# Kernel tuning notes

Hardware: AMD Instinct MI355X
Metric: run time of the kernel (lower is better)

Reference implementation:

```python
import jax, jax.numpy as jnp
import numpy as np

K = 20          # neighbors
EPS = 1e-5      # BatchNorm eps
SLOPE = 0.2     # LeakyReLU negative slope


def setup_inputs() -> dict:
    key = jax.random.key(0)
    k1, k2 = jax.random.split(key)
    B, C, N, O = 8, 64, 4096, 64
    x = jax.random.normal(k1, (B, C, N), dtype=jnp.float32)
    # 1x1 Conv2d(2C -> O, bias=False) kernel, squeezed to (O, 2C)
    W = jax.random.normal(k2, (O, 2 * C), dtype=jnp.float32) * 0.05
    gamma = jnp.ones((O,), jnp.float32)   # BN weight
    beta = jnp.zeros((O,), jnp.float32)   # BN bias
    return {"x": x, "W": W, "gamma": gamma, "beta": beta}


def _edgeconv(x, W, gamma, beta):
    B, C, N = x.shape
    xt = jnp.transpose(x, (0, 2, 1))                       # (B, N, C)
    # KNN on negative squared distance (matches torch topk of -dist)
    xx = jnp.sum(x * x, axis=1)                            # (B, N)
    inner = jnp.einsum('bnc,bmc->bnm', xt, xt)             # (B, N, N)
    neg_dist = 2.0 * inner - xx[:, :, None] - xx[:, None, :]
    _, idx = jax.lax.top_k(neg_dist, K)                    # (B, N, K) int32
    # gather neighbor features: nbr[b,n,k,c] = xt[b, idx[b,n,k], c]
    nbr = xt[jnp.arange(B)[:, None, None], idx]            # (B, N, K, C)
    center = jnp.broadcast_to(xt[:, :, None, :], (B, N, K, C))
    edge = jnp.concatenate([nbr - center, center], axis=-1)  # (B, N, K, 2C)
    # 1x1 conv == channel matmul
    y = jnp.einsum('bnkc,oc->bnko', edge, W)               # (B, N, K, O)
    # BatchNorm2d (training mode: batch statistics over B,N,K per channel)
    mean = jnp.mean(y, axis=(0, 1, 2))
    var = jnp.var(y, axis=(0, 1, 2))
    yn = (y - mean) * jax.lax.rsqrt(var + EPS) * gamma + beta
    ya = jnp.where(yn >= 0, yn, SLOPE * yn)                # LeakyReLU(0.2)
    out = jnp.max(ya, axis=2)                              # max over k -> (B, N, O)
    return jnp.transpose(out, (0, 2, 1))                   # (B, O, N)


def reference(x, W, gamma, beta):
    return _edgeconv(x, W, gamma, beta)
```

## Files before the change

### kernel.cpp

```cpp
#include <hip/hip_runtime.h>
#include <hip/hip_bf16.h>
#include <math.h>

#define B 8
#define C 64
#define NN 4096
#define O 64
#define KNN 20

typedef float f32x4 __attribute__((ext_vector_type(4)));
typedef short short8_t __attribute__((ext_vector_type(8)));

__device__ inline uint32_t fkey(float f) {
    uint32_t u = __float_as_uint(f);
    return u ^ (((uint32_t)((int32_t)u >> 31)) | 0x80000000u);
}

__device__ inline uint32_t med3u(uint32_t a, uint32_t b, uint32_t c) {
    uint32_t r;
    asm("v_med3_u32 %0, %1, %2, %3" : "=v"(r) : "v"(a), "v"(b), "v"(c));
    return r;
}
__device__ inline uint32_t umax(uint32_t a, uint32_t b) { return a > b ? a : b; }
__device__ inline uint32_t umin(uint32_t a, uint32_t b) { return a < b ? a : b; }

__device__ inline uint32_t maxall16(uint32_t v) {
    uint32_t t;
    t = (uint32_t)__builtin_amdgcn_update_dpp(0, (int)v, 0x140, 0xF, 0xF, true);
    v = umax(v, t);
    t = (uint32_t)__builtin_amdgcn_update_dpp(0, (int)v, 0x141, 0xF, 0xF, true);
    v = umax(v, t);
    t = (uint32_t)__builtin_amdgcn_update_dpp(0, (int)v, 0x4E, 0xF, 0xF, true);
    v = umax(v, t);
    t = (uint32_t)__builtin_amdgcn_update_dpp(0, (int)v, 0xB1, 0xF, 0xF, true);
    v = umax(v, t);
    return v;
}
__device__ inline uint32_t minall16(uint32_t v) {
    uint32_t t;
    t = (uint32_t)__builtin_amdgcn_update_dpp(0, (int)v, 0x140, 0xF, 0xF, true);
    v = umin(v, t);
    t = (uint32_t)__builtin_amdgcn_update_dpp(0, (int)v, 0x141, 0xF, 0xF, true);
    v = umin(v, t);
    t = (uint32_t)__builtin_amdgcn_update_dpp(0, (int)v, 0x4E, 0xF, 0xF, true);
    v = umin(v, t);
    t = (uint32_t)__builtin_amdgcn_update_dpp(0, (int)v, 0xB1, 0xF, 0xF, true);
    v = umin(v, t);
    return v;
}

__global__ __launch_bounds__(256) void k1_split(const float* __restrict__ x,
                                                float* __restrict__ xt,
                                                __hip_bfloat16* __restrict__ xh,
                                                float* __restrict__ xx) {
    __shared__ float tile[64][65];
    int b  = blockIdx.x / (NN / 64);
    int n0 = (blockIdx.x % (NN / 64)) * 64;
    int t = threadIdx.x;
    #pragma unroll
    for (int it = 0; it < 16; ++it) {
        int i = it * 256 + t;
        int c = i >> 6, n = i & 63;
        tile[c][n] = x[(size_t)b * C * NN + (size_t)c * NN + n0 + n];
    }
    __syncthreads();
    #pragma unroll
    for (int it = 0; it < 16; ++it) {
        int i = it * 256 + t;
        int n = i >> 6, c = i & 63;
        float v = tile[c][n];
        size_t off = ((size_t)(b * NN + n0 + n)) * C + c;
        xt[off] = v;
        xh[off] = __float2bfloat16(v);
    }
    if (t < 64) {
        float s = 0.f;
        #pragma unroll
        for (int c = 0; c < 64; ++c) { float v = tile[c][t]; s = fmaf(v, v, s); }
        xx[(size_t)b * NN + t + n0] = s;
    }
}

__global__ __launch_bounds__(256) void k2_knn(const __hip_bfloat16* __restrict__ xh,
                                              const float* __restrict__ xt,
                                              const float* __restrict__ xx,
                                              int* __restrict__ idx) {
    int b  = blockIdx.x & 7;
    int n0 = (blockIdx.x >> 3) << 4;
    int t = threadIdx.x;
    int w = t >> 6, lane = t & 63;
    int laneid = lane & 15, grp = lane >> 4;

    const __hip_bfloat16* xhb = xh + (size_t)b * NN * 64;
    const float* xxb = xx + (size_t)b * NN;
    const float* xtb = xt + (size_t)b * NN * 64;

    size_t qoff = (size_t)(n0 + laneid) * 64 + grp * 8;
    short8_t Ah0 = *(const short8_t*)(xhb + qoff);
    short8_t Ah1 = *(const short8_t*)(xhb + qoff + 32);

    float bq[4];
    #pragma unroll
    for (int j = 0; j < 4; ++j) bq[j] = -2.f - xxb[n0 + grp * 4 + j];

    uint32_t qq[4][12];
    #pragma unroll
    for (int j = 0; j < 4; ++j)
        #pragma unroll
        for (int i = 0; i < 12; ++i) qq[j][i] = 0xFFFFFFFFu;

    int cand0 = w * 1024 + laneid;
    {
        const __hip_bfloat16* p0 = xhb + (size_t)cand0 * 64 + grp * 8;
        short8_t nB0 = *(const short8_t*)p0;
        short8_t nB1 = *(const short8_t*)(p0 + 32);
        float nxx = xxb[cand0];
        #pragma unroll 4
        for (int tt = 0; tt < 64; ++tt) {
            short8_t B0 = nB0, B1 = nB1;
            float xxc = nxx;
            int ci = cand0 + tt * 16;
            {
                const __hip_bfloat16* np = xhb + (size_t)(ci + 16) * 64 + grp * 8;
                nB0 = *(const short8_t*)np;
                nB1 = *(const short8_t*)(np + 32);
                nxx = xxb[ci + 16];
            }
            f32x4 acc = {0.f, 0.f, 0.f, 0.f};
            acc = __builtin_amdgcn_mfma_f32_16x16x32_bf16(Ah0, B0, acc, 0, 0, 0);
            acc = __builtin_amdgcn_mfma_f32_16x16x32_bf16(Ah1, B1, acc, 0, 0, 0);
            #pragma unroll
            for (int j = 0; j < 4; ++j) {
                uint32_t u = __float_as_uint(fmaf(acc[j], 2.f, bq[j] - xxc));
                uint32_t nv = (u & 0xFFFFF000u) | (uint32_t)ci;
                #pragma unroll
                for (int i = 11; i >= 1; --i)
                    qq[j][i] = med3u(qq[j][i - 1], qq[j][i], nv);
                qq[j][0] = umin(qq[j][0], nv);
            }
        }
    }

    __shared__ uint32_t mbuf[16][4][20];
    __shared__ uint32_t cand[16][33];
    __shared__ uint32_t rkk[16][33];
    __shared__ float qrow[16][68];

    #pragma unroll
    for (int i = 0; i < 4; ++i) {
        int e = i * 256 + t;
        int r = e >> 6, cc = e & 63;
        qrow[r][cc] = xtb[(size_t)(n0 + r) * 64 + cc];
    }

    #pragma unroll 1
    for (int r = 0; r < 20; ++r) {
        #pragma unroll
        for (int j = 0; j < 4; ++j) {
            uint32_t bk = minall16(qq[j][0]);
            bool win = (qq[j][0] == bk);
            #pragma unroll
            for (int i = 0; i < 11; ++i) qq[j][i] = win ? qq[j][i + 1] : qq[j][i];
            qq[j][11] = win ? 0xFFFFFFFFu : qq[j][11];
            if (laneid == 0) mbuf[grp * 4 + j][w][r] = bk;
        }
    }
    __syncthreads();

    {
        int q = w * 4 + grp;
        const uint32_t* mb = &mbuf[q][0][0];
        uint32_t e0 = mb[laneid],      e1 = mb[16 + laneid], e2 = mb[32 + laneid],
                 e3 = mb[48 + laneid], e4 = mb[64 + laneid];
        #pragma unroll 1
        for (int r = 0; r < 32; ++r) {
            uint32_t bk = umin(umin(umin(e0, e1), umin(e2, e3)), e4);
            bk = minall16(bk);
            e0 = (e0 == bk) ? 0xFFFFFFFFu : e0;
            e1 = (e1 == bk) ? 0xFFFFFFFFu : e1;
            e2 = (e2 == bk) ? 0xFFFFFFFFu : e2;
            e3 = (e3 == bk) ? 0xFFFFFFFFu : e3;
            e4 = (e4 == bk) ? 0xFFFFFFFFu : e4;
            if (laneid == 0) cand[q][r] = bk & 4095u;
        }
    }
    __syncthreads();

    int rq = t >> 4, rs = t & 15;
    float qxx = xxb[n0 + rq];
    const float4* qr = (const float4*)qrow[rq];
    uint32_t mycol[2], mykey[2];
    #pragma unroll
    for (int e = 0; e < 2; ++e) {
        uint32_t col = cand[rq][rs + 16 * e];
        const float4* cr = (const float4*)(xtb + (size_t)col * 64);
        float a = 0.f;
        #pragma unroll
        for (int i = 0; i < 16; ++i) {
            float4 qv = qr[i], cv = cr[i];
            a = fmaf(qv.x, cv.x, a); a = fmaf(qv.y, cv.y, a);
            a = fmaf(qv.z, cv.z, a); a = fmaf(qv.w, cv.w, a);
        }
        float d = 2.f * a - qxx - xxb[col];
        mycol[e] = col;
        mykey[e] = fkey(d);
        rkk[rq][rs + 16 * e] = mykey[e];
    }
    __syncthreads();
    size_t ob = ((size_t)(b * NN) + n0 + rq) * KNN;
    #pragma unroll
    for (int e = 0; e < 2; ++e) {
        uint32_t ke = mykey[e], ce = mycol[e];
        int rank = 0;
        #pragma unroll
        for (int jj = 0; jj < 32; ++jj) {
            uint32_t kj = rkk[rq][jj], cj = cand[rq][jj];
            rank += (kj > ke || (kj == ke && cj < ce)) ? 1 : 0;
        }
        if (rank < KNN) idx[ob + rank] = (int)ce;
    }
}

__global__ __launch_bounds__(256) void k3a_gemm(const float* __restrict__ xt,
                                                const float* __restrict__ W,
                                                float* __restrict__ Z,
                                                float* __restrict__ Z2) {
    __shared__ float W0t[64][65];
    __shared__ float W21t[64][65];
    __shared__ float xs[16][64];
    int t = threadIdx.x;
    #pragma unroll
    for (int it = 0; it < 16; ++it) {
        int i = it * 256 + t;
        int o = i >> 6, c = i & 63;
        float w0 = W[o * 128 + c];
        float w1 = W[o * 128 + 64 + c];
        W0t[c][o]  = w0;
        W21t[c][o] = w1 - w0;
    }
    int b  = blockIdx.x / (NN / 16);
    int nb = (blockIdx.x % (NN / 16)) * 16;
    #pragma unroll
    for (int it = 0; it < 4; ++it) {
        int i = it * 256 + t;
        int r = i >> 6, c = i & 63;
        xs[r][c] = xt[((size_t)(b * NN + nb + r)) * C + c];
    }
    __syncthreads();
    int o = t & 63, rg = t >> 6;
    #pragma unroll
    for (int rr = 0; rr < 4; ++rr) {
        int r = rg * 4 + rr;
        float z = 0.f, z2 = 0.f;
        #pragma unroll
        for (int c = 0; c < 64; ++c) {
            float xv = xs[r][c];
            z  = fmaf(xv, W0t[c][o],  z);
            z2 = fmaf(xv, W21t[c][o], z2);
        }
        size_t off = ((size_t)(b * NN + nb + r)) * 64 + o;
        Z[off]  = z;
        Z2[off] = z2;
    }
}

__global__ __launch_bounds__(256) void k3b_gather(const float* __restrict__ Z,
                                                  const float* __restrict__ Z2,
                                                  const int* __restrict__ idx,
                                                  float* __restrict__ maxY,
                                                  float* __restrict__ minY,
                                                  float* __restrict__ partials) {
    int t = threadIdx.x;
    int p = t >> 6, o = t & 63;
    int b = blockIdx.x & 7;
    int n = (blockIdx.x >> 3) * 4 + p;
    size_t base = (size_t)(b * NN + n);
    float z2 = Z2[base * 64 + o];
    __shared__ int sidx[4][KNN];
    if (o < KNN) sidx[p][o] = idx[base * KNN + o];
    __syncthreads();
    const float* Zb = Z + (size_t)b * NN * 64;
    float s1 = 0.f, s2 = 0.f, mx = -INFINITY, mn = INFINITY;
    #pragma unroll
    for (int k = 0; k < KNN; ++k) {
        float y = Zb[(size_t)sidx[p][k] * 64 + o] + z2;
        s1 += y;
        s2 = fmaf(y, y, s2);
        mx = fmaxf(mx, y);
        mn = fminf(mn, y);
    }
    maxY[base * 64 + o] = mx;
    minY[base * 64 + o] = mn;
    __shared__ float red[2][4][64];
    red[0][p][o] = s1;
    red[1][p][o] = s2;
    __syncthreads();
    if (t < 64) {
        float a = red[0][0][t] + red[0][1][t] + red[0][2][t] + red[0][3][t];
        float c = red[1][0][t] + red[1][1][t] + red[1][2][t] + red[1][3][t];
        partials[(size_t)blockIdx.x * 128 + t]      = a;
        partials[(size_t)blockIdx.x * 128 + 64 + t] = c;
    }
}

__global__ __launch_bounds__(256) void k4a_reduce(const float* __restrict__ partials,
                                                  float* __restrict__ partials2) {
    int g = blockIdx.x;
    int t = threadIdx.x;
    int col = t & 127, half = t >> 7;
    float s = 0.f;
    for (int r = half; r < 128; r += 2)
        s += partials[((size_t)g * 128 + r) * 128 + col];
    __shared__ float red[2][128];
    red[half][col] = s;
    __syncthreads();
    if (t < 128) partials2[(size_t)g * 128 + t] = red[0][t] + red[1][t];
}

__global__ __launch_bounds__(128) void k4b_stats(const float* __restrict__ partials2,
                                                 const float* __restrict__ gamma,
                                                 const float* __restrict__ beta,
                                                 float* __restrict__ ss) {
    int t = threadIdx.x;
    double s = 0.0;
    for (int i = 0; i < 64; ++i)
        s += (double)partials2[(size_t)i * 128 + t];
    __shared__ double red[128];
    red[t] = s;
    __syncthreads();
    if (t < 64) {
        double a = red[t], c = red[64 + t];
        double M = (double)B * NN * KNN;
        double mean = a / M;
        double var  = c / M - mean * mean;
        float sc = gamma[t] * rsqrtf((float)var + 1e-5f);
        float sh = beta[t] - (float)mean * sc;
        ss[t]      = sc;
        ss[64 + t] = sh;
    }
}

__global__ __launch_bounds__(256) void k5_out(const float* __restrict__ maxY,
                                              const float* __restrict__ minY,
                                              const float* __restrict__ ss,
                                              float* __restrict__ out) {
    __shared__ float tile[64][65];
    __shared__ float sc[64], sh[64];
    int t = threadIdx.x;
    if (t < 64) { sc[t] = ss[t]; sh[t] = ss[64 + t]; }
    int b  = blockIdx.x / (NN / 64);
    int n0 = (blockIdx.x % (NN / 64)) * 64;
    __syncthreads();
    #pragma unroll
    for (int it = 0; it < 16; ++it) {
        int i = it * 256 + t;
        int nl = i >> 6, o = i & 63;
        size_t off = ((size_t)(b * NN + n0 + nl)) * 64 + o;
        float s = sc[o];
        float v = (s >= 0.f) ? maxY[off] : minY[off];
        v = fmaf(v, s, sh[o]);
        v = (v >= 0.f) ? v : 0.2f * v;
        tile[nl][o] = v;
    }
    __syncthreads();
    #pragma unroll
    for (int it = 0; it < 16; ++it) {
        int i = it * 256 + t;
        int o = i >> 6, nl = i & 63;
        out[((size_t)(b * O + o)) * NN + n0 + nl] = tile[nl][o];
    }
}

extern "C" void kernel_launch(void* const* d_in, const int* in_sizes, int n_in,
                              void* d_out, int out_size, void* d_ws, size_t ws_size,
                              hipStream_t stream) {
    const float* x     = (const float*)d_in[0];
    const float* W     = (const float*)d_in[1];
    const float* gamma = (const float*)d_in[2];
    const float* beta  = (const float*)d_in[3];
    float* out = (float*)d_out;

    float* ws = (float*)d_ws;
    float* xx = ws;
    float* xt = xx + (size_t)B * NN;
    __hip_bfloat16* xh = (__hip_bfloat16*)(xt + (size_t)B * NN * C);
    int*   idx = (int*)(xh + (size_t)B * NN * C);
    float* Z   = (float*)(idx + (size_t)B * NN * KNN);
    float* Z2  = Z + (size_t)B * NN * O;
    float* maxY = Z2 + (size_t)B * NN * O;
    float* minY = maxY + (size_t)B * NN * O;
    float* partials  = minY + (size_t)B * NN * O;
    float* partials2 = partials + (size_t)(B * NN / 4) * 128;
    float* ss = partials2 + 64 * 128;

    k1_split<<<B * (NN / 64), 256, 0, stream>>>(x, xt, xh, xx);
    k2_knn<<<B * (NN / 16), 256, 0, stream>>>(xh, xt, xx, idx);
    k3a_gemm<<<B * (NN / 16), 256, 0, stream>>>(xt, W, Z, Z2);
    k3b_gather<<<B * (NN / 4), 256, 0, stream>>>(Z, Z2, idx, maxY, minY, partials);
    k4a_reduce<<<64, 256, 0, stream>>>(partials, partials2);
    k4b_stats<<<1, 128, 0, stream>>>(partials2, gamma, beta, ss);
    k5_out<<<B * (NN / 64), 256, 0, stream>>>(maxY, minY, ss, out);
}
```

Baseline: 256.2 us.

## Give each KNN wave its own queries over all candidates, dropping cross-wave merge

The KNN kernel now assigns 16 queries to each wave, and each wave scans all 4096 candidates. Before, the 4 waves of a block split the candidates for a shared set of 16 queries and then merged their partial lists through shared memory. The merge stage and one block barrier go away, the grid shrinks to 64 queries per block, and the candidate sweep keeps four chunks in flight instead of one. The rerank is reworked so 4 lanes handle each query with 8 candidates each. In exchange there are four times fewer blocks, each running longer, which may lower occupancy and latency hiding.

```diff
diff --git a/kernel.cpp b/kernel.cpp
--- a/kernel.cpp
+++ b/kernel.cpp
@@ -24,18 +24,6 @@
 __device__ inline uint32_t umax(uint32_t a, uint32_t b) { return a > b ? a : b; }
 __device__ inline uint32_t umin(uint32_t a, uint32_t b) { return a < b ? a : b; }
 
-__device__ inline uint32_t maxall16(uint32_t v) {
-    uint32_t t;
-    t = (uint32_t)__builtin_amdgcn_update_dpp(0, (int)v, 0x140, 0xF, 0xF, true);
-    v = umax(v, t);
-    t = (uint32_t)__builtin_amdgcn_update_dpp(0, (int)v, 0x141, 0xF, 0xF, true);
-    v = umax(v, t);
-    t = (uint32_t)__builtin_amdgcn_update_dpp(0, (int)v, 0x4E, 0xF, 0xF, true);
-    v = umax(v, t);
-    t = (uint32_t)__builtin_amdgcn_update_dpp(0, (int)v, 0xB1, 0xF, 0xF, true);
-    v = umax(v, t);
-    return v;
-}
 __device__ inline uint32_t minall16(uint32_t v) {
     uint32_t t;
     t = (uint32_t)__builtin_amdgcn_update_dpp(0, (int)v, 0x140, 0xF, 0xF, true);
@@ -85,23 +73,24 @@
                                               const float* __restrict__ xt,
                                               const float* __restrict__ xx,
                                               int* __restrict__ idx) {
-    int b  = blockIdx.x & 7;
-    int n0 = (blockIdx.x >> 3) << 4;
+    int b     = blockIdx.x & 7;
+    int qbase = (blockIdx.x >> 3) << 6;
     int t = threadIdx.x;
     int w = t >> 6, lane = t & 63;
     int laneid = lane & 15, grp = lane >> 4;
+    int n0w = qbase + w * 16;
 
     const __hip_bfloat16* xhb = xh + (size_t)b * NN * 64;
     const float* xxb = xx + (size_t)b * NN;
     const float* xtb = xt + (size_t)b * NN * 64;
 
-    size_t qoff = (size_t)(n0 + laneid) * 64 + grp * 8;
+    size_t qoff = (size_t)(n0w + laneid) * 64 + grp * 8;
     short8_t Ah0 = *(const short8_t*)(xhb + qoff);
     short8_t Ah1 = *(const short8_t*)(xhb + qoff + 32);
 
     float bq[4];
     #pragma unroll
-    for (int j = 0; j < 4; ++j) bq[j] = -2.f - xxb[n0 + grp * 4 + j];
+    for (int j = 0; j < 4; ++j) bq[j] = -2.f - xxb[n0w + grp * 4 + j];
 
     uint32_t qq[4][12];
     #pragma unroll
@@ -109,52 +98,58 @@
         #pragma unroll
         for (int i = 0; i < 12; ++i) qq[j][i] = 0xFFFFFFFFu;
 
-    int cand0 = w * 1024 + laneid;
-    {
-        const __hip_bfloat16* p0 = xhb + (size_t)cand0 * 64 + grp * 8;
-        short8_t nB0 = *(const short8_t*)p0;
-        short8_t nB1 = *(const short8_t*)(p0 + 32);
-        float nxx = xxb[cand0];
-        #pragma unroll 4
-        for (int tt = 0; tt < 64; ++tt) {
-            short8_t B0 = nB0, B1 = nB1;
-            float xxc = nxx;
-            int ci = cand0 + tt * 16;
-            {
-                const __hip_bfloat16* np = xhb + (size_t)(ci + 16) * 64 + grp * 8;
-                nB0 = *(const short8_t*)np;
-                nB1 = *(const short8_t*)(np + 32);
-                nxx = xxb[ci + 16];
-            }
-            f32x4 acc = {0.f, 0.f, 0.f, 0.f};
-            acc = __builtin_amdgcn_mfma_f32_16x16x32_bf16(Ah0, B0, acc, 0, 0, 0);
-            acc = __builtin_amdgcn_mfma_f32_16x16x32_bf16(Ah1, B1, acc, 0, 0, 0);
-            #pragma unroll
-            for (int j = 0; j < 4; ++j) {
-                uint32_t u = __float_as_uint(fmaf(acc[j], 2.f, bq[j] - xxc));
-                uint32_t nv = (u & 0xFFFFF000u) | (uint32_t)ci;
-                #pragma unroll
-                for (int i = 11; i >= 1; --i)
-                    qq[j][i] = med3u(qq[j][i - 1], qq[j][i], nv);
-                qq[j][0] = umin(qq[j][0], nv);
-            }
-        }
-    }
-
-    __shared__ uint32_t mbuf[16][4][20];
-    __shared__ uint32_t cand[16][33];
-    __shared__ uint32_t rkk[16][33];
-    __shared__ float qrow[16][68];
-
-    #pragma unroll
-    for (int i = 0; i < 4; ++i) {
-        int e = i * 256 + t;
-        int r = e >> 6, cc = e & 63;
-        qrow[r][cc] = xtb[(size_t)(n0 + r) * 64 + cc];
+    const __hip_bfloat16* blp = xhb + (size_t)laneid * 64 + grp * 8;
+    short8_t P00, P01, P10, P11, P20, P21, P30, P31;
+    float Px0, Px1, Px2, Px3;
+    P00 = *(const short8_t*)(blp);            P01 = *(const short8_t*)(blp + 32);
+    P10 = *(const short8_t*)(blp + 1024);     P11 = *(const short8_t*)(blp + 1024 + 32);
+    P20 = *(const short8_t*)(blp + 2048);     P21 = *(const short8_t*)(blp + 2048 + 32);
+    P30 = *(const short8_t*)(blp + 3072);     P31 = *(const short8_t*)(blp + 3072 + 32);
+    Px0 = xxb[laneid];      Px1 = xxb[laneid + 16];
+    Px2 = xxb[laneid + 32]; Px3 = xxb[laneid + 48];
+
+#define SWEEP_BODY(PB0, PB1, PXX, K)                                           \
+    {                                                                          \
+        float xxc = PXX;                                                       \
+        f32x4 acc = {0.f, 0.f, 0.f, 0.f};                                      \
+        acc = __builtin_amdgcn_mfma_f32_16x16x32_bf16(Ah0, PB0, acc, 0, 0, 0); \
+        acc = __builtin_amdgcn_mfma_f32_16x16x32_bf16(Ah1, PB1, acc, 0, 0, 0); \
+        const __hip_bfloat16* np = blp + (size_t)(tt + 4 + K) * 1024;          \
+        PB0 = *(const short8_t*)np;                                            \
+        PB1 = *(const short8_t*)(np + 32);                                     \
+        PXX = xxb[ci0 + (4 + K) * 16];                                         \
+        uint32_t ci = (uint32_t)(ci0 + K * 16);                                \
+        _Pragma("unroll")                                                      \
+        for (int j = 0; j < 4; ++j) {                                          \
+            uint32_t u = __float_as_uint(fmaf(acc[j], 2.f, bq[j] - xxc));      \
+            uint32_t nv = (u & 0xFFFFF000u) | ci;                              \
+            _Pragma("unroll")                                                  \
+            for (int i = 11; i >= 1; --i)                                      \
+                qq[j][i] = med3u(qq[j][i - 1], qq[j][i], nv);                  \
+            qq[j][0] = umin(qq[j][0], nv);                                     \
+        }                                                                      \
     }
 
     #pragma unroll 1
-    for (int r = 0; r < 20; ++r) {
+    for (int tt = 0; tt < 256; tt += 4) {
+        int ci0 = tt * 16 + laneid;
+        SWEEP_BODY(P00, P01, Px0, 0)
+        SWEEP_BODY(P10, P11, Px1, 1)
+        SWEEP_BODY(P20, P21, Px2, 2)
+        SWEEP_BODY(P30, P31, Px3, 3)
+    }
+#undef SWEEP_BODY
+
+    __shared__ uint32_t cand[4][16][33];
+    __shared__ uint32_t rkk[4][16][33];
+    __shared__ float qrow[4][16][68];
+
+    #pragma unroll
+    for (int i = 0; i < 16; ++i)
+        qrow[w][i][lane] = xtb[(size_t)(n0w + i) * 64 + lane];
+
+    #pragma unroll 1
+    for (int r = 0; r < 32; ++r) {
         #pragma unroll
         for (int j = 0; j < 4; ++j) {
             uint32_t bk = minall16(qq[j][0]);
@@ -162,37 +157,18 @@
             #pragma unroll
             for (int i = 0; i < 11; ++i) qq[j][i] = win ? qq[j][i + 1] : qq[j][i];
             qq[j][11] = win ? 0xFFFFFFFFu : qq[j][11];
-            if (laneid == 0) mbuf[grp * 4 + j][w][r] = bk;
+            if (laneid == 0) cand[w][grp * 4 + j][r] = bk & 4095u;
         }
     }
     __syncthreads();
 
-    {
-        int q = w * 4 + grp;
-        const uint32_t* mb = &mbuf[q][0][0];
-        uint32_t e0 = mb[laneid],      e1 = mb[16 + laneid], e2 = mb[32 + laneid],
-                 e3 = mb[48 + laneid], e4 = mb[64 + laneid];
-        #pragma unroll 1
-        for (int r = 0; r < 32; ++r) {
-            uint32_t bk = umin(umin(umin(e0, e1), umin(e2, e3)), e4);
-            bk = minall16(bk);
-            e0 = (e0 == bk) ? 0xFFFFFFFFu : e0;
-            e1 = (e1 == bk) ? 0xFFFFFFFFu : e1;
-            e2 = (e2 == bk) ? 0xFFFFFFFFu : e2;
-            e3 = (e3 == bk) ? 0xFFFFFFFFu : e3;
-            e4 = (e4 == bk) ? 0xFFFFFFFFu : e4;
-            if (laneid == 0) cand[q][r] = bk & 4095u;
-        }
-    }
-    __syncthreads();
-
-    int rq = t >> 4, rs = t & 15;
-    float qxx = xxb[n0 + rq];
-    const float4* qr = (const float4*)qrow[rq];
-    uint32_t mycol[2], mykey[2];
-    #pragma unroll
-    for (int e = 0; e < 2; ++e) {
-        uint32_t col = cand[rq][rs + 16 * e];
+    int rq = lane >> 2, rs = lane & 3;
+    float qxx = xxb[n0w + rq];
+    const float4* qr = (const float4*)qrow[w][rq];
+    uint32_t ky[8], cl[8];
+    #pragma unroll
+    for (int e = 0; e < 8; ++e) {
+        uint32_t col = cand[w][rq][rs + 4 * e];
         const float4* cr = (const float4*)(xtb + (size_t)col * 64);
         float a = 0.f;
         #pragma unroll
@@ -202,23 +178,26 @@
             a = fmaf(qv.z, cv.z, a); a = fmaf(qv.w, cv.w, a);
         }
         float d = 2.f * a - qxx - xxb[col];
-        mycol[e] = col;
-        mykey[e] = fkey(d);
-        rkk[rq][rs + 16 * e] = mykey[e];
-    }
-    __syncthreads();
-    size_t ob = ((size_t)(b * NN) + n0 + rq) * KNN;
-    #pragma unroll
-    for (int e = 0; e < 2; ++e) {
-        uint32_t ke = mykey[e], ce = mycol[e];
-        int rank = 0;
-        #pragma unroll
-        for (int jj = 0; jj < 32; ++jj) {
-            uint32_t kj = rkk[rq][jj], cj = cand[rq][jj];
-            rank += (kj > ke || (kj == ke && cj < ce)) ? 1 : 0;
-        }
-        if (rank < KNN) idx[ob + rank] = (int)ce;
-    }
+        ky[e] = fkey(d);
+        cl[e] = col;
+        rkk[w][rq][rs + 4 * e] = ky[e];
+    }
+    __syncthreads();
+
+    int rank[8];
+    #pragma unroll
+    for (int e = 0; e < 8; ++e) rank[e] = 0;
+    #pragma unroll
+    for (int jj = 0; jj < 32; ++jj) {
+        uint32_t kj = rkk[w][rq][jj], cj = cand[w][rq][jj];
+        #pragma unroll
+        for (int e = 0; e < 8; ++e)
+            rank[e] += (kj > ky[e] || (kj == ky[e] && cj < cl[e])) ? 1 : 0;
+    }
+    size_t ob = ((size_t)(b * NN) + n0w + rq) * KNN;
+    #pragma unroll
+    for (int e = 0; e < 8; ++e)
+        if (rank[e] < KNN) idx[ob + rank[e]] = (int)cl[e];
 }
 
 __global__ __launch_bounds__(256) void k3a_gemm(const float* __restrict__ xt,
@@ -394,7 +373,7 @@
     float* ss = partials2 + 64 * 128;
 
     k1_split<<<B * (NN / 64), 256, 0, stream>>>(x, xt, xh, xx);
-    k2_knn<<<B * (NN / 16), 256, 0, stream>>>(xh, xt, xx, idx);
+    k2_knn<<<B * (NN / 64), 256, 0, stream>>>(xh, xt, xx, idx);
     k3a_gemm<<<B * (NN / 16), 256, 0, stream>>>(xt, W, Z, Z2);
     k3b_gather<<<B * (NN / 4), 256, 0, stream>>>(Z, Z2, idx, maxY, minY, partials);
     k4a_reduce<<<64, 256, 0, stream>>>(partials, partials2);
```

After: 255.3 us. Within noise of the previous version (-0.3%).
